# Kernel optimization log

Hardware: AMD Instinct MI355X
Metric: run time of the kernel (lower is better)

The kernel has to match this reference:

```python
import jax, jax.numpy as jnp
import numpy as np

N_NODES = 100000
N_EDGES = 1600000
BN_EPS = 1e-5

def gin_layer(h, src, dst, eps, w1, b1, w2, b2, gamma, beta, mean, var):
    # message passing: sum of source-node features at each target node
    agg = jax.ops.segment_sum(h[src], dst, num_segments=h.shape[0])  # [N, H]
    z = (1.0 + eps) * h + agg
    z = jax.nn.relu(z @ w1 + b1)
    z = jax.nn.relu(z @ w2 + b2)
    # BatchNorm1d in eval mode (running stats as params)
    return gamma * (z - mean) * jax.lax.rsqrt(var + BN_EPS) + beta

def setup_inputs() -> dict:
    key = jax.random.key(0)
    ks = jax.random.split(key, 12)
    H = 64
    s = lambda fan: 1.0 / np.sqrt(fan)
    inp = {
        "x": jax.random.normal(ks[0], (N_NODES, 128), jnp.float32),
        "edge_index": jax.random.randint(ks[1], (2, N_EDGES), 0, N_NODES, jnp.int64),
        "eps": jnp.zeros((3,), jnp.float32),
        "c1_w1": jax.random.normal(ks[2], (128, H), jnp.float32) * s(128),
        "c1_b1": jnp.zeros((H,), jnp.float32),
        "c1_w2": jax.random.normal(ks[3], (H, H), jnp.float32) * s(H),
        "c1_b2": jnp.zeros((H,), jnp.float32),
        "c1_gamma": jnp.ones((H,), jnp.float32),
        "c1_beta": jnp.zeros((H,), jnp.float32),
        "c1_mean": jnp.zeros((H,), jnp.float32),
        "c1_var": jnp.ones((H,), jnp.float32),
        "cw1": jax.random.normal(ks[4], (2, H, H), jnp.float32) * s(H),
        "cb1": jnp.zeros((2, H), jnp.float32),
        "cw2": jax.random.normal(ks[5], (2, H, H), jnp.float32) * s(H),
        "cb2": jnp.zeros((2, H), jnp.float32),
        "cgamma": jnp.ones((2, H), jnp.float32),
        "cbeta": jnp.zeros((2, H), jnp.float32),
        "cmean": jnp.zeros((2, H), jnp.float32),
        "cvar": jnp.ones((2, H), jnp.float32),
        "lin1_w": jax.random.normal(ks[6], (H, H), jnp.float32) * s(H),
        "lin1_b": jnp.zeros((H,), jnp.float32),
        "lin2_w": jax.random.normal(ks[7], (H, 40), jnp.float32) * s(H),
        "lin2_b": jnp.zeros((40,), jnp.float32),
    }
    return inp

def reference(x, edge_index, eps, c1_w1, c1_b1, c1_w2, c1_b2, c1_gamma, c1_beta,
              c1_mean, c1_var, cw1, cb1, cw2, cb2, cgamma, cbeta, cmean, cvar,
              lin1_w, lin1_b, lin2_w, lin2_b):
    src, dst = edge_index[0], edge_index[1]
    h = gin_layer(x, src, dst, eps[0], c1_w1, c1_b1, c1_w2, c1_b2,
                  c1_gamma, c1_beta, c1_mean, c1_var)
    for i in range(2):  # num_layers - 1 stacked GINConvs
        h = gin_layer(h, src, dst, eps[i + 1], cw1[i], cb1[i], cw2[i], cb2[i],
                      cgamma[i], cbeta[i], cmean[i], cvar[i])
    h = jax.nn.relu(h @ lin1_w + lin1_b)
    # dropout(p=0.5) is identity in eval mode
    return h @ lin2_w + lin2_b  # logits [N, num_classes]
```

## Files before the change

kernel.cpp:

```cpp
#include <hip/hip_runtime.h>

#define NN 100000
#define NE 1600000
#define BN_EPS 1e-5f
#define NCOARSE 98
#define SC_CH 2048

typedef unsigned int u32;
typedef unsigned short u16;

static constexpr size_t OFF_ROW  = 0;
static constexpr size_t OFF_CTRL = 512u * 1024;
static constexpr size_t OFF_CSR  = 1u << 20;
static constexpr size_t OFF_U    = 8u << 20;
static constexpr size_t OFF_P1   = OFF_U;
static constexpr size_t OFF_YB0  = OFF_U + (size_t)NN * 64 * 4;
static constexpr size_t OFF_YB1  = OFF_YB0 + (size_t)NN * 64 * 2;

__device__ __forceinline__ u16 f2bf(float f) {
  u32 u = __float_as_uint(f);
  return (u16)((u + 0x7fffu + ((u >> 16) & 1u)) >> 16);
}
__device__ __forceinline__ float bflo(u32 u) { return __uint_as_float(u << 16); }
__device__ __forceinline__ float bfhi(u32 u) { return __uint_as_float(u & 0xffff0000u); }
__device__ __forceinline__ u32 pkbf(float lo, float hi) {
  return (u32)f2bf(lo) | ((u32)f2bf(hi) << 16);
}

typedef __bf16 bf16x8 __attribute__((ext_vector_type(8)));
typedef float f32x4 __attribute__((ext_vector_type(4)));
union FragCvt { uint4 u; bf16x8 b; u16 s[8]; };
__device__ __forceinline__ bf16x8 frag_u16(const u16* p) {
  FragCvt c; c.u = *(const uint4*)p; return c.b;
}

__global__ void __launch_bounds__(256) k_hist_c(const int* __restrict__ dst,
                                                int* __restrict__ ch) {
  __shared__ int h[NCOARSE];
  if (threadIdx.x < NCOARSE) h[threadIdx.x] = 0;
  __syncthreads();
  int i = blockIdx.x * 256 + threadIdx.x, stride = gridDim.x * 256;
  for (; i < NE; i += stride) atomicAdd(&h[dst[i] >> 10], 1);
  __syncthreads();
  if (threadIdx.x < NCOARSE && h[threadIdx.x]) atomicAdd(&ch[threadIdx.x], h[threadIdx.x]);
}

__global__ void k_scan_c(const int* __restrict__ ch, int* __restrict__ coff,
                         int* __restrict__ ccur) {
  if (threadIdx.x == 0) {
    int acc = 0;
    for (int i = 0; i < NCOARSE; i++) { coff[i] = acc; ccur[i] = acc; acc += ch[i]; }
    coff[NCOARSE] = acc;
  }
}

__global__ void __launch_bounds__(256) k_scat1(const int* __restrict__ src,
                                               const int* __restrict__ dst,
                                               int* __restrict__ ccur,
                                               u32* __restrict__ pairs1) {
  __shared__ int h[NCOARSE], base[NCOARSE];
  int t = threadIdx.x;
  int e0 = blockIdx.x * SC_CH;
  if (t < NCOARSE) h[t] = 0;
  __syncthreads();
  int myc[8]; u32 mypk[8];
#pragma unroll
  for (int q = 0; q < 8; q++) {
    int e = e0 + q * 256 + t;
    if (e < NE) {
      int d = dst[e], s = src[e];
      myc[q] = d >> 10;
      mypk[q] = (u32)s | ((u32)(d & 1023) << 17);
      atomicAdd(&h[myc[q]], 1);
    } else myc[q] = -1;
  }
  __syncthreads();
  if (t < NCOARSE) {
    base[t] = (h[t] > 0) ? atomicAdd(&ccur[t], h[t]) : 0;
    h[t] = 0;
  }
  __syncthreads();
#pragma unroll
  for (int q = 0; q < 8; q++) {
    if (myc[q] >= 0) {
      int p = atomicAdd(&h[myc[q]], 1);
      pairs1[base[myc[q]] + p] = mypk[q];
    }
  }
}

__global__ void __launch_bounds__(256) k_fill3(const u32* __restrict__ pairs1,
                                               const int* __restrict__ coff,
                                               int* __restrict__ row,
                                               int* __restrict__ csr) {
  __shared__ int lcnt[1024];
  __shared__ int loff[1024];
  __shared__ int sd[256];
  __shared__ u32 stage[20480];
  int c = blockIdx.x, t = threadIdx.x;
  int es = coff[c], ee = coff[c + 1];
  int m = ee - es;
  int nbase = c << 10;
  int nodes_in = NN - nbase; if (nodes_in > 1024) nodes_in = 1024;
  for (int i = t; i < 1024; i += 256) lcnt[i] = 0;
  __syncthreads();
  for (int i = es + t; i < ee; i += 256)
    atomicAdd(&lcnt[(pairs1[i] >> 17) & 1023], 1);
  __syncthreads();
  int b4 = t * 4;
  int c0 = lcnt[b4], c1 = lcnt[b4 + 1], c2 = lcnt[b4 + 2], c3 = lcnt[b4 + 3];
  int s4 = c0 + c1 + c2 + c3;
  sd[t] = s4;
  __syncthreads();
  for (int o = 1; o < 256; o <<= 1) {
    int x = (t >= o) ? sd[t - o] : 0;
    __syncthreads();
    sd[t] += x;
    __syncthreads();
  }
  int run = sd[t] - s4;
  loff[b4] = run;     run += c0;
  loff[b4 + 1] = run; run += c1;
  loff[b4 + 2] = run; run += c2;
  loff[b4 + 3] = run;
  __syncthreads();
  for (int i = t; i < nodes_in; i += 256) row[nbase + i] = es + loff[i];
  if (c == NCOARSE - 1 && t == 0) row[NN] = NE;
  for (int i = t; i < 1024; i += 256) lcnt[i] = loff[i];
  __syncthreads();
  if (m <= 20480) {
    for (int i = es + t; i < ee; i += 256) {
      u32 pk = pairs1[i];
      int p = atomicAdd(&lcnt[(pk >> 17) & 1023], 1);
      stage[p] = pk & 0x1FFFFu;
    }
    __syncthreads();
    for (int i = t; i < m; i += 256) csr[es + i] = (int)stage[i];
  } else {
    for (int i = es + t; i < ee; i += 256) {
      u32 pk = pairs1[i];
      int p = atomicAdd(&lcnt[(pk >> 17) & 1023], 1);
      csr[es + p] = (int)(pk & 0x1FFFFu);
    }
  }
}

__global__ void __launch_bounds__(256) k_gemm_x_mfma(const float* __restrict__ x,
                                                     const float* __restrict__ w,
                                                     u16* __restrict__ yb) {
  __shared__ __align__(16) u16 wT[64][136];
  __shared__ __align__(16) u16 ht[4][32][72];
  int tid = threadIdx.x;
  for (int idx = tid; idx < 8192; idx += 256) {
    int k = idx >> 6, n = idx & 63;
    wT[n][k] = f2bf(w[idx]);
  }
  __syncthreads();
  int wid = tid >> 6, lane = tid & 63;
  int grp = blockIdx.x * 4 + wid;
  if (grp >= NN / 32) return;
  int g0 = grp * 32;
  int mrow = lane & 15;
  int kc8 = (lane >> 4) * 8;
  int q4 = (lane >> 4) * 4;
  bf16x8 a[2][4];
#pragma unroll
  for (int mt = 0; mt < 2; mt++) {
    const float* xr = x + (size_t)(g0 + mt * 16 + mrow) * 128;
#pragma unroll
    for (int kc = 0; kc < 4; kc++) {
      float4 v0 = *(const float4*)(xr + kc * 32 + kc8);
      float4 v1 = *(const float4*)(xr + kc * 32 + kc8 + 4);
      FragCvt fc;
      fc.s[0] = f2bf(v0.x); fc.s[1] = f2bf(v0.y); fc.s[2] = f2bf(v0.z); fc.s[3] = f2bf(v0.w);
      fc.s[4] = f2bf(v1.x); fc.s[5] = f2bf(v1.y); fc.s[6] = f2bf(v1.z); fc.s[7] = f2bf(v1.w);
      a[mt][kc] = fc.b;
    }
  }
  f32x4 zero = {0.f, 0.f, 0.f, 0.f};
  f32x4 acc[2][4];
#pragma unroll
  for (int nt = 0; nt < 4; nt++) {
    bf16x8 bf[4];
#pragma unroll
    for (int kc = 0; kc < 4; kc++)
      bf[kc] = frag_u16(&wT[nt * 16 + mrow][kc * 32 + kc8]);
#pragma unroll
    for (int mt = 0; mt < 2; mt++) {
      f32x4 c = __builtin_amdgcn_mfma_f32_16x16x32_bf16(a[mt][0], bf[0], zero, 0, 0, 0);
      c = __builtin_amdgcn_mfma_f32_16x16x32_bf16(a[mt][1], bf[1], c, 0, 0, 0);
      c = __builtin_amdgcn_mfma_f32_16x16x32_bf16(a[mt][2], bf[2], c, 0, 0, 0);
      c = __builtin_amdgcn_mfma_f32_16x16x32_bf16(a[mt][3], bf[3], c, 0, 0, 0);
      acc[mt][nt] = c;
    }
  }
#pragma unroll
  for (int mt = 0; mt < 2; mt++)
#pragma unroll
    for (int nt = 0; nt < 4; nt++)
#pragma unroll
      for (int r = 0; r < 4; r++)
        ht[wid][mt * 16 + q4 + r][nt * 16 + mrow] = f2bf(acc[mt][nt][r]);
  asm volatile("s_waitcnt lgkmcnt(0)" ::: "memory");
#pragma unroll
  for (int it = 0; it < 4; it++) {
    int idx = it * 64 + lane;
    int rw = idx >> 3, ch = idx & 7;
    uint4 v = *(const uint4*)&ht[wid][rw][ch * 8];
    *(uint4*)(yb + (size_t)(g0 + rw) * 64 + ch * 8) = v;
  }
}

__global__ void __launch_bounds__(256) k_agg(
    const u16* __restrict__ yb, const int* __restrict__ row, const int* __restrict__ csr,
    const float* __restrict__ epsv, int ei, const float* __restrict__ b1,
    u16* __restrict__ ub) {
  int t = blockIdx.x * 256 + threadIdx.x;
  int n = t >> 3, g = t & 7;
  if (n >= NN) return;
  const u16* bp = yb + g * 8;
  float a0 = 0, a1 = 0, a2 = 0, a3 = 0, a4 = 0, a5 = 0, a6 = 0, a7 = 0;
  int rs = row[n], re = row[n + 1];
  int i = rs;
  for (; i + 8 <= re; i += 8) {
    uint4 v[8];
#pragma unroll
    for (int q = 0; q < 8; q++) {
      int s = csr[i + q];
      v[q] = *(const uint4*)(bp + (size_t)s * 64);
    }
#pragma unroll
    for (int q = 0; q < 8; q++) {
      a0 += bflo(v[q].x); a1 += bfhi(v[q].x); a2 += bflo(v[q].y); a3 += bfhi(v[q].y);
      a4 += bflo(v[q].z); a5 += bfhi(v[q].z); a6 += bflo(v[q].w); a7 += bfhi(v[q].w);
    }
  }
  for (; i + 4 <= re; i += 4) {
    uint4 v[4];
#pragma unroll
    for (int q = 0; q < 4; q++) {
      int s = csr[i + q];
      v[q] = *(const uint4*)(bp + (size_t)s * 64);
    }
#pragma unroll
    for (int q = 0; q < 4; q++) {
      a0 += bflo(v[q].x); a1 += bfhi(v[q].x); a2 += bflo(v[q].y); a3 += bfhi(v[q].y);
      a4 += bflo(v[q].z); a5 += bfhi(v[q].z); a6 += bflo(v[q].w); a7 += bfhi(v[q].w);
    }
  }
  for (; i < re; ++i) {
    int s = csr[i];
    uint4 v0 = *(const uint4*)(bp + (size_t)s * 64);
    a0 += bflo(v0.x); a1 += bfhi(v0.x); a2 += bflo(v0.y); a3 += bfhi(v0.y);
    a4 += bflo(v0.z); a5 += bfhi(v0.z); a6 += bflo(v0.w); a7 += bfhi(v0.w);
  }
  uint4 sv = *(const uint4*)(bp + (size_t)n * 64);
  float e1 = 1.0f + epsv[ei];
  const float* bb = b1 + g * 8;
  float r0 = fmaxf(fmaf(e1, bflo(sv.x), a0 + bb[0]), 0.f);
  float r1 = fmaxf(fmaf(e1, bfhi(sv.x), a1 + bb[1]), 0.f);
  float r2 = fmaxf(fmaf(e1, bflo(sv.y), a2 + bb[2]), 0.f);
  float r3 = fmaxf(fmaf(e1, bfhi(sv.y), a3 + bb[3]), 0.f);
  float r4 = fmaxf(fmaf(e1, bflo(sv.z), a4 + bb[4]), 0.f);
  float r5 = fmaxf(fmaf(e1, bfhi(sv.z), a5 + bb[5]), 0.f);
  float r6 = fmaxf(fmaf(e1, bflo(sv.w), a6 + bb[6]), 0.f);
  float r7 = fmaxf(fmaf(e1, bfhi(sv.w), a7 + bb[7]), 0.f);
  uint4 pk;
  pk.x = pkbf(r0, r1); pk.y = pkbf(r2, r3);
  pk.z = pkbf(r4, r5); pk.w = pkbf(r6, r7);
  *(uint4*)(ub + (size_t)n * 64 + g * 8) = pk;
}

__global__ void __launch_bounds__(256) k_mlp_mfma(
    const u16* __restrict__ ub, const float* __restrict__ w2, const float* __restrict__ b2,
    const float* __restrict__ gamma, const float* __restrict__ beta,
    const float* __restrict__ mean, const float* __restrict__ var,
    const float* __restrict__ wn, u16* __restrict__ yout) {
  __shared__ __align__(16) u16 w2T[64][72];
  __shared__ __align__(16) u16 wnT[64][72];
  __shared__ __align__(16) u16 ht[4][32][72];
  int tid = threadIdx.x;
  for (int idx = tid; idx < 4096; idx += 256) {
    int k = idx >> 6, n = idx & 63;
    w2T[n][k] = f2bf(w2[idx]);
    wnT[n][k] = f2bf(wn[idx]);
  }
  __syncthreads();
  int wid = tid >> 6, lane = tid & 63;
  int grp = blockIdx.x * 4 + wid;
  if (grp >= NN / 32) return;
  int g0 = grp * 32;
  int mrow = lane & 15;
  int kc8 = (lane >> 4) * 8;
  int q4 = (lane >> 4) * 4;
  float bb[4], gl[4], be[4], mn[4], rv[4];
#pragma unroll
  for (int nt = 0; nt < 4; nt++) {
    int j = nt * 16 + mrow;
    bb[nt] = b2[j]; gl[nt] = gamma[j]; be[nt] = beta[j]; mn[nt] = mean[j];
    rv[nt] = rsqrtf(var[j] + BN_EPS);
  }
  bf16x8 a[2][2];
#pragma unroll
  for (int mt = 0; mt < 2; mt++)
#pragma unroll
    for (int kc = 0; kc < 2; kc++)
      a[mt][kc] = frag_u16(ub + (size_t)(g0 + mt * 16 + mrow) * 64 + kc * 32 + kc8);
  f32x4 zero = {0.f, 0.f, 0.f, 0.f};
  f32x4 acc[2][4];
#pragma unroll
  for (int nt = 0; nt < 4; nt++) {
    bf16x8 b0 = frag_u16(&w2T[nt * 16 + mrow][kc8]);
    bf16x8 b1f = frag_u16(&w2T[nt * 16 + mrow][32 + kc8]);
#pragma unroll
    for (int mt = 0; mt < 2; mt++) {
      acc[mt][nt] = __builtin_amdgcn_mfma_f32_16x16x32_bf16(a[mt][0], b0, zero, 0, 0, 0);
      acc[mt][nt] = __builtin_amdgcn_mfma_f32_16x16x32_bf16(a[mt][1], b1f, acc[mt][nt], 0, 0, 0);
    }
  }
#pragma unroll
  for (int mt = 0; mt < 2; mt++)
#pragma unroll
    for (int nt = 0; nt < 4; nt++)
#pragma unroll
      for (int r = 0; r < 4; r++) {
        float v = fmaxf(acc[mt][nt][r] + bb[nt], 0.f);
        float h = fmaf(gl[nt] * (v - mn[nt]), rv[nt], be[nt]);
        ht[wid][mt * 16 + q4 + r][nt * 16 + mrow] = f2bf(h);
      }
  asm volatile("s_waitcnt lgkmcnt(0)" ::: "memory");
  bf16x8 a2[2][2];
#pragma unroll
  for (int mt = 0; mt < 2; mt++)
#pragma unroll
    for (int kc = 0; kc < 2; kc++)
      a2[mt][kc] = frag_u16(&ht[wid][mt * 16 + mrow][kc * 32 + kc8]);
  f32x4 ac2[2][4];
#pragma unroll
  for (int nt = 0; nt < 4; nt++) {
    bf16x8 b0 = frag_u16(&wnT[nt * 16 + mrow][kc8]);
    bf16x8 b1f = frag_u16(&wnT[nt * 16 + mrow][32 + kc8]);
#pragma unroll
    for (int mt = 0; mt < 2; mt++) {
      ac2[mt][nt] = __builtin_amdgcn_mfma_f32_16x16x32_bf16(a2[mt][0], b0, zero, 0, 0, 0);
      ac2[mt][nt] = __builtin_amdgcn_mfma_f32_16x16x32_bf16(a2[mt][1], b1f, ac2[mt][nt], 0, 0, 0);
    }
  }
  asm volatile("s_waitcnt lgkmcnt(0)" ::: "memory");
#pragma unroll
  for (int mt = 0; mt < 2; mt++)
#pragma unroll
    for (int nt = 0; nt < 4; nt++)
#pragma unroll
      for (int r = 0; r < 4; r++)
        ht[wid][mt * 16 + q4 + r][nt * 16 + mrow] = f2bf(ac2[mt][nt][r]);
  asm volatile("s_waitcnt lgkmcnt(0)" ::: "memory");
#pragma unroll
  for (int it = 0; it < 4; it++) {
    int idx = it * 64 + lane;
    int rw = idx >> 3, ch = idx & 7;
    uint4 v = *(const uint4*)&ht[wid][rw][ch * 8];
    *(uint4*)(yout + (size_t)(g0 + rw) * 64 + ch * 8) = v;
  }
}

__global__ void __launch_bounds__(256) k_mlp_final_mfma(
    const u16* __restrict__ ub, const float* __restrict__ w2, const float* __restrict__ b2,
    const float* __restrict__ gamma, const float* __restrict__ beta,
    const float* __restrict__ mean, const float* __restrict__ var,
    const float* __restrict__ l1w, const float* __restrict__ l1b,
    const float* __restrict__ l2w, const float* __restrict__ l2b,
    float* __restrict__ out) {
  __shared__ __align__(16) u16 w2T[64][72];
  __shared__ __align__(16) u16 l1T[64][72];
  __shared__ __align__(16) u16 l2T[48][72];
  __shared__ __align__(16) u16 ht[4][32][72];
  int tid = threadIdx.x;
  for (int idx = tid; idx < 4096; idx += 256) {
    int k = idx >> 6, n = idx & 63;
    w2T[n][k] = f2bf(w2[idx]);
    l1T[n][k] = f2bf(l1w[idx]);
  }
  for (int idx = tid; idx < 3072; idx += 256) {
    int n = idx >> 6, k = idx & 63;
    l2T[n][k] = f2bf((n < 40) ? l2w[k * 40 + n] : 0.f);
  }
  __syncthreads();
  int wid = tid >> 6, lane = tid & 63;
  int grp = blockIdx.x * 4 + wid;
  if (grp >= NN / 32) return;
  int g0 = grp * 32;
  int mrow = lane & 15;
  int kc8 = (lane >> 4) * 8;
  int q4 = (lane >> 4) * 4;
  float bb[4], gl[4], be[4], mn[4], rv[4], l1bv[4];
#pragma unroll
  for (int nt = 0; nt < 4; nt++) {
    int j = nt * 16 + mrow;
    bb[nt] = b2[j]; gl[nt] = gamma[j]; be[nt] = beta[j]; mn[nt] = mean[j];
    rv[nt] = rsqrtf(var[j] + BN_EPS); l1bv[nt] = l1b[j];
  }
  float l2bv[3];
#pragma unroll
  for (int nt = 0; nt < 3; nt++) {
    int j = nt * 16 + mrow;
    l2bv[nt] = (j < 40) ? l2b[j] : 0.f;
  }
  bf16x8 a[2][2];
#pragma unroll
  for (int mt = 0; mt < 2; mt++)
#pragma unroll
    for (int kc = 0; kc < 2; kc++)
      a[mt][kc] = frag_u16(ub + (size_t)(g0 + mt * 16 + mrow) * 64 + kc * 32 + kc8);
  f32x4 zero = {0.f, 0.f, 0.f, 0.f};
  f32x4 acc[2][4];
#pragma unroll
  for (int nt = 0; nt < 4; nt++) {
    bf16x8 b0 = frag_u16(&w2T[nt * 16 + mrow][kc8]);
    bf16x8 b1f = frag_u16(&w2T[nt * 16 + mrow][32 + kc8]);
#pragma unroll
    for (int mt = 0; mt < 2; mt++) {
      acc[mt][nt] = __builtin_amdgcn_mfma_f32_16x16x32_bf16(a[mt][0], b0, zero, 0, 0, 0);
      acc[mt][nt] = __builtin_amdgcn_mfma_f32_16x16x32_bf16(a[mt][1], b1f, acc[mt][nt], 0, 0, 0);
    }
  }
#pragma unroll
  for (int mt = 0; mt < 2; mt++)
#pragma unroll
    for (int nt = 0; nt < 4; nt++)
#pragma unroll
      for (int r = 0; r < 4; r++) {
        float v = fmaxf(acc[mt][nt][r] + bb[nt], 0.f);
        float h = fmaf(gl[nt] * (v - mn[nt]), rv[nt], be[nt]);
        ht[wid][mt * 16 + q4 + r][nt * 16 + mrow] = f2bf(h);
      }
  asm volatile("s_waitcnt lgkmcnt(0)" ::: "memory");
  bf16x8 a2[2][2];
#pragma unroll
  for (int mt = 0; mt < 2; mt++)
#pragma unroll
    for (int kc = 0; kc < 2; kc++)
      a2[mt][kc] = frag_u16(&ht[wid][mt * 16 + mrow][kc * 32 + kc8]);
  f32x4 ac2[2][4];
#pragma unroll
  for (int nt = 0; nt < 4; nt++) {
    bf16x8 b0 = frag_u16(&l1T[nt * 16 + mrow][kc8]);
    bf16x8 b1f = frag_u16(&l1T[nt * 16 + mrow][32 + kc8]);
#pragma unroll
    for (int mt = 0; mt < 2; mt++) {
      ac2[mt][nt] = __builtin_amdgcn_mfma_f32_16x16x32_bf16(a2[mt][0], b0, zero, 0, 0, 0);
      ac2[mt][nt] = __builtin_amdgcn_mfma_f32_16x16x32_bf16(a2[mt][1], b1f, ac2[mt][nt], 0, 0, 0);
    }
  }
  asm volatile("s_waitcnt lgkmcnt(0)" ::: "memory");
#pragma unroll
  for (int mt = 0; mt < 2; mt++)
#pragma unroll
    for (int nt = 0; nt < 4; nt++)
#pragma unroll
      for (int r = 0; r < 4; r++) {
        float f = fmaxf(ac2[mt][nt][r] + l1bv[nt], 0.f);
        ht[wid][mt * 16 + q4 + r][nt * 16 + mrow] = f2bf(f);
      }
  asm volatile("s_waitcnt lgkmcnt(0)" ::: "memory");
  bf16x8 a3[2][2];
#pragma unroll
  for (int mt = 0; mt < 2; mt++)
#pragma unroll
    for (int kc = 0; kc < 2; kc++)
      a3[mt][kc] = frag_u16(&ht[wid][mt * 16 + mrow][kc * 32 + kc8]);
  f32x4 ac3[2][3];
#pragma unroll
  for (int nt = 0; nt < 3; nt++) {
    bf16x8 b0 = frag_u16(&l2T[nt * 16 + mrow][kc8]);
    bf16x8 b1f = frag_u16(&l2T[nt * 16 + mrow][32 + kc8]);
#pragma unroll
    for (int mt = 0; mt < 2; mt++) {
      ac3[mt][nt] = __builtin_amdgcn_mfma_f32_16x16x32_bf16(a3[mt][0], b0, zero, 0, 0, 0);
      ac3[mt][nt] = __builtin_amdgcn_mfma_f32_16x16x32_bf16(a3[mt][1], b1f, ac3[mt][nt], 0, 0, 0);
    }
  }
#pragma unroll
  for (int mt = 0; mt < 2; mt++)
#pragma unroll
    for (int nt = 0; nt < 3; nt++) {
      int j = nt * 16 + mrow;
      if (j < 40) {
#pragma unroll
        for (int r = 0; r < 4; r++)
          out[(size_t)(g0 + mt * 16 + q4 + r) * 40 + j] = ac3[mt][nt][r] + l2bv[nt];
      }
    }
}

extern "C" void kernel_launch(void* const* d_in, const int* in_sizes, int n_in,
                              void* d_out, int out_size, void* d_ws, size_t ws_size,
                              hipStream_t stream) {
  const float* x   = (const float*)d_in[0];
  const int*   ei  = (const int*)d_in[1];
  const int*   src = ei;
  const int*   dst = ei + NE;
  const float* eps = (const float*)d_in[2];
  const float* c1_w1 = (const float*)d_in[3];
  const float* c1_b1 = (const float*)d_in[4];
  const float* c1_w2 = (const float*)d_in[5];
  const float* c1_b2 = (const float*)d_in[6];
  const float* c1_gamma = (const float*)d_in[7];
  const float* c1_beta  = (const float*)d_in[8];
  const float* c1_mean  = (const float*)d_in[9];
  const float* c1_var   = (const float*)d_in[10];
  const float* cw1 = (const float*)d_in[11];
  const float* cb1 = (const float*)d_in[12];
  const float* cw2 = (const float*)d_in[13];
  const float* cb2 = (const float*)d_in[14];
  const float* cgamma = (const float*)d_in[15];
  const float* cbeta  = (const float*)d_in[16];
  const float* cmean  = (const float*)d_in[17];
  const float* cvar   = (const float*)d_in[18];
  const float* lin1_w = (const float*)d_in[19];
  const float* lin1_b = (const float*)d_in[20];
  const float* lin2_w = (const float*)d_in[21];
  const float* lin2_b = (const float*)d_in[22];
  float* out = (float*)d_out;

  char* ws = (char*)d_ws;
  int* row  = (int*)(ws + OFF_ROW);
  int* ctrl = (int*)(ws + OFF_CTRL);
  int* ch   = ctrl;
  int* coff = ctrl + 128;
  int* ccur = ctrl + 256;
  int* csr  = (int*)(ws + OFF_CSR);
  u32* pairs1 = (u32*)(ws + OFF_P1);
  u16* ubuf = (u16*)(ws + OFF_U);
  u16* yb0  = (u16*)(ws + OFF_YB0);
  u16* yb1  = (u16*)(ws + OFF_YB1);

  hipMemsetAsync(ch, 0, NCOARSE * 4, stream);

  k_hist_c<<<512, 256, 0, stream>>>(dst, ch);
  k_scan_c<<<1, 64, 0, stream>>>(ch, coff, ccur);
  k_scat1<<<(NE + SC_CH - 1) / SC_CH, 256, 0, stream>>>(src, dst, ccur, pairs1);
  k_fill3<<<NCOARSE, 256, 0, stream>>>(pairs1, coff, row, csr);

  const int AGG_GRID = (NN * 8) / 256;
  const int MLP_GRID = (NN / 32 + 3) / 4;

  k_gemm_x_mfma<<<MLP_GRID, 256, 0, stream>>>(x, c1_w1, yb0);

  k_agg<<<AGG_GRID, 256, 0, stream>>>(yb0, row, csr, eps, 0, c1_b1, ubuf);
  k_mlp_mfma<<<MLP_GRID, 256, 0, stream>>>(ubuf, c1_w2, c1_b2,
                                           c1_gamma, c1_beta, c1_mean, c1_var,
                                           cw1, yb1);
  k_agg<<<AGG_GRID, 256, 0, stream>>>(yb1, row, csr, eps, 1, cb1, ubuf);
  k_mlp_mfma<<<MLP_GRID, 256, 0, stream>>>(ubuf, cw2, cb2,
                                           cgamma, cbeta, cmean, cvar,
                                           cw1 + 64 * 64, yb0);
  k_agg<<<AGG_GRID, 256, 0, stream>>>(yb0, row, csr, eps, 2, cb1 + 64, ubuf);
  k_mlp_final_mfma<<<MLP_GRID, 256, 0, stream>>>(ubuf, cw2 + 64 * 64, cb2 + 64,
                                                 cgamma + 64, cbeta + 64, cmean + 64, cvar + 64,
                                                 lin1_w, lin1_b, lin2_w, lin2_b,
                                                 out);
}
```

Baseline: 233.5 us.

## Fuse neighbor aggregation with per-layer MLP into a single GIN kernel

Merges the separate aggregation and MLP kernels into one kernel per layer. Each block gathers neighbor sums for 64 nodes into shared memory, then runs the two MFMA GEMMs with bias, ReLU and batch-norm on that tile. This removes the intermediate bf16 buffer round-trip through global memory and three kernel launches. In exchange each thread now gathers 16 features instead of 8, which means fewer threads per node and more registers per thread, and every block repeats the weight transpose into shared memory.

```diff
diff --git a/kernel.cpp b/kernel.cpp
--- a/kernel.cpp
+++ b/kernel.cpp
@@ -12,9 +12,8 @@
 static constexpr size_t OFF_ROW  = 0;
 static constexpr size_t OFF_CTRL = 512u * 1024;
 static constexpr size_t OFF_CSR  = 1u << 20;
-static constexpr size_t OFF_U    = 8u << 20;
-static constexpr size_t OFF_P1   = OFF_U;
-static constexpr size_t OFF_YB0  = OFF_U + (size_t)NN * 64 * 4;
+static constexpr size_t OFF_P1   = 8u << 20;
+static constexpr size_t OFF_YB0  = OFF_P1 + (size_t)NN * 64 * 4;
 static constexpr size_t OFF_YB1  = OFF_YB0 + (size_t)NN * 64 * 2;
 
 __device__ __forceinline__ u16 f2bf(float f) {
@@ -211,193 +210,301 @@
   }
 }
 
-__global__ void __launch_bounds__(256) k_agg(
+__global__ void __launch_bounds__(256, 4) k_gin_layer(
     const u16* __restrict__ yb, const int* __restrict__ row, const int* __restrict__ csr,
     const float* __restrict__ epsv, int ei, const float* __restrict__ b1,
-    u16* __restrict__ ub) {
-  int t = blockIdx.x * 256 + threadIdx.x;
-  int n = t >> 3, g = t & 7;
-  if (n >= NN) return;
-  const u16* bp = yb + g * 8;
-  float a0 = 0, a1 = 0, a2 = 0, a3 = 0, a4 = 0, a5 = 0, a6 = 0, a7 = 0;
-  int rs = row[n], re = row[n + 1];
-  int i = rs;
-  for (; i + 8 <= re; i += 8) {
-    uint4 v[8];
-#pragma unroll
-    for (int q = 0; q < 8; q++) {
-      int s = csr[i + q];
-      v[q] = *(const uint4*)(bp + (size_t)s * 64);
-    }
-#pragma unroll
-    for (int q = 0; q < 8; q++) {
-      a0 += bflo(v[q].x); a1 += bfhi(v[q].x); a2 += bflo(v[q].y); a3 += bfhi(v[q].y);
-      a4 += bflo(v[q].z); a5 += bfhi(v[q].z); a6 += bflo(v[q].w); a7 += bfhi(v[q].w);
-    }
-  }
-  for (; i + 4 <= re; i += 4) {
-    uint4 v[4];
-#pragma unroll
-    for (int q = 0; q < 4; q++) {
-      int s = csr[i + q];
-      v[q] = *(const uint4*)(bp + (size_t)s * 64);
-    }
-#pragma unroll
-    for (int q = 0; q < 4; q++) {
-      a0 += bflo(v[q].x); a1 += bfhi(v[q].x); a2 += bflo(v[q].y); a3 += bfhi(v[q].y);
-      a4 += bflo(v[q].z); a5 += bfhi(v[q].z); a6 += bflo(v[q].w); a7 += bfhi(v[q].w);
-    }
-  }
-  for (; i < re; ++i) {
-    int s = csr[i];
-    uint4 v0 = *(const uint4*)(bp + (size_t)s * 64);
-    a0 += bflo(v0.x); a1 += bfhi(v0.x); a2 += bflo(v0.y); a3 += bfhi(v0.y);
-    a4 += bflo(v0.z); a5 += bfhi(v0.z); a6 += bflo(v0.w); a7 += bfhi(v0.w);
-  }
-  uint4 sv = *(const uint4*)(bp + (size_t)n * 64);
-  float e1 = 1.0f + epsv[ei];
-  const float* bb = b1 + g * 8;
-  float r0 = fmaxf(fmaf(e1, bflo(sv.x), a0 + bb[0]), 0.f);
-  float r1 = fmaxf(fmaf(e1, bfhi(sv.x), a1 + bb[1]), 0.f);
-  float r2 = fmaxf(fmaf(e1, bflo(sv.y), a2 + bb[2]), 0.f);
-  float r3 = fmaxf(fmaf(e1, bfhi(sv.y), a3 + bb[3]), 0.f);
-  float r4 = fmaxf(fmaf(e1, bflo(sv.z), a4 + bb[4]), 0.f);
-  float r5 = fmaxf(fmaf(e1, bfhi(sv.z), a5 + bb[5]), 0.f);
-  float r6 = fmaxf(fmaf(e1, bflo(sv.w), a6 + bb[6]), 0.f);
-  float r7 = fmaxf(fmaf(e1, bfhi(sv.w), a7 + bb[7]), 0.f);
-  uint4 pk;
-  pk.x = pkbf(r0, r1); pk.y = pkbf(r2, r3);
-  pk.z = pkbf(r4, r5); pk.w = pkbf(r6, r7);
-  *(uint4*)(ub + (size_t)n * 64 + g * 8) = pk;
-}
-
-__global__ void __launch_bounds__(256) k_mlp_mfma(
-    const u16* __restrict__ ub, const float* __restrict__ w2, const float* __restrict__ b2,
+    const float* __restrict__ w2, const float* __restrict__ b2,
     const float* __restrict__ gamma, const float* __restrict__ beta,
     const float* __restrict__ mean, const float* __restrict__ var,
     const float* __restrict__ wn, u16* __restrict__ yout) {
-  __shared__ __align__(16) u16 w2T[64][72];
-  __shared__ __align__(16) u16 wnT[64][72];
-  __shared__ __align__(16) u16 ht[4][32][72];
+  __shared__ __align__(16) u16 wA[64][72];
+  __shared__ __align__(16) u16 wB[64][72];
+  __shared__ __align__(16) u16 buf[64][72];
   int tid = threadIdx.x;
   for (int idx = tid; idx < 4096; idx += 256) {
     int k = idx >> 6, n = idx & 63;
-    w2T[n][k] = f2bf(w2[idx]);
-    wnT[n][k] = f2bf(wn[idx]);
-  }
-  __syncthreads();
-  int wid = tid >> 6, lane = tid & 63;
-  int grp = blockIdx.x * 4 + wid;
-  if (grp >= NN / 32) return;
-  int g0 = grp * 32;
-  int mrow = lane & 15;
-  int kc8 = (lane >> 4) * 8;
-  int q4 = (lane >> 4) * 4;
-  float bb[4], gl[4], be[4], mn[4], rv[4];
+    wA[n][k] = f2bf(w2[idx]);
+    wB[n][k] = f2bf(wn[idx]);
+  }
+  __syncthreads();
+
+  int ln = tid >> 2, q = tid & 3;
+  int n = blockIdx.x * 64 + ln;
+  int fb = q * 16;
+  float a[16];
+#pragma unroll
+  for (int j = 0; j < 16; j++) a[j] = 0.f;
+  if (n < NN) {
+    const u16* bp = yb + fb;
+    int rs = row[n], re = row[n + 1];
+    int i = rs;
+    for (; i + 8 <= re; i += 8) {
+      uint4 v[16];
+#pragma unroll
+      for (int p = 0; p < 8; p++) {
+        const u16* rp = bp + (size_t)csr[i + p] * 64;
+        v[2 * p]     = *(const uint4*)rp;
+        v[2 * p + 1] = *(const uint4*)(rp + 8);
+      }
+#pragma unroll
+      for (int p = 0; p < 8; p++) {
+        uint4 v0 = v[2 * p], v1 = v[2 * p + 1];
+        a[0] += bflo(v0.x); a[1] += bfhi(v0.x); a[2] += bflo(v0.y); a[3] += bfhi(v0.y);
+        a[4] += bflo(v0.z); a[5] += bfhi(v0.z); a[6] += bflo(v0.w); a[7] += bfhi(v0.w);
+        a[8] += bflo(v1.x); a[9] += bfhi(v1.x); a[10] += bflo(v1.y); a[11] += bfhi(v1.y);
+        a[12] += bflo(v1.z); a[13] += bfhi(v1.z); a[14] += bflo(v1.w); a[15] += bfhi(v1.w);
+      }
+    }
+    for (; i + 4 <= re; i += 4) {
+      uint4 v[8];
+#pragma unroll
+      for (int p = 0; p < 4; p++) {
+        const u16* rp = bp + (size_t)csr[i + p] * 64;
+        v[2 * p]     = *(const uint4*)rp;
+        v[2 * p + 1] = *(const uint4*)(rp + 8);
+      }
+#pragma unroll
+      for (int p = 0; p < 4; p++) {
+        uint4 v0 = v[2 * p], v1 = v[2 * p + 1];
+        a[0] += bflo(v0.x); a[1] += bfhi(v0.x); a[2] += bflo(v0.y); a[3] += bfhi(v0.y);
+        a[4] += bflo(v0.z); a[5] += bfhi(v0.z); a[6] += bflo(v0.w); a[7] += bfhi(v0.w);
+        a[8] += bflo(v1.x); a[9] += bfhi(v1.x); a[10] += bflo(v1.y); a[11] += bfhi(v1.y);
+        a[12] += bflo(v1.z); a[13] += bfhi(v1.z); a[14] += bflo(v1.w); a[15] += bfhi(v1.w);
+      }
+    }
+    for (; i < re; ++i) {
+      const u16* rp = bp + (size_t)csr[i] * 64;
+      uint4 v0 = *(const uint4*)rp;
+      uint4 v1 = *(const uint4*)(rp + 8);
+      a[0] += bflo(v0.x); a[1] += bfhi(v0.x); a[2] += bflo(v0.y); a[3] += bfhi(v0.y);
+      a[4] += bflo(v0.z); a[5] += bfhi(v0.z); a[6] += bflo(v0.w); a[7] += bfhi(v0.w);
+      a[8] += bflo(v1.x); a[9] += bfhi(v1.x); a[10] += bflo(v1.y); a[11] += bfhi(v1.y);
+      a[12] += bflo(v1.z); a[13] += bfhi(v1.z); a[14] += bflo(v1.w); a[15] += bfhi(v1.w);
+    }
+    const u16* sp = yb + (size_t)n * 64 + fb;
+    uint4 s0 = *(const uint4*)sp, s1 = *(const uint4*)(sp + 8);
+    float e1 = 1.0f + epsv[ei];
+    float4 bb0 = *(const float4*)(b1 + fb);
+    float4 bb1 = *(const float4*)(b1 + fb + 4);
+    float4 bb2 = *(const float4*)(b1 + fb + 8);
+    float4 bb3 = *(const float4*)(b1 + fb + 12);
+    float r[16];
+    r[0] = fmaxf(fmaf(e1, bflo(s0.x), a[0] + bb0.x), 0.f);
+    r[1] = fmaxf(fmaf(e1, bfhi(s0.x), a[1] + bb0.y), 0.f);
+    r[2] = fmaxf(fmaf(e1, bflo(s0.y), a[2] + bb0.z), 0.f);
+    r[3] = fmaxf(fmaf(e1, bfhi(s0.y), a[3] + bb0.w), 0.f);
+    r[4] = fmaxf(fmaf(e1, bflo(s0.z), a[4] + bb1.x), 0.f);
+    r[5] = fmaxf(fmaf(e1, bfhi(s0.z), a[5] + bb1.y), 0.f);
+    r[6] = fmaxf(fmaf(e1, bflo(s0.w), a[6] + bb1.z), 0.f);
+    r[7] = fmaxf(fmaf(e1, bfhi(s0.w), a[7] + bb1.w), 0.f);
+    r[8] = fmaxf(fmaf(e1, bflo(s1.x), a[8] + bb2.x), 0.f);
+    r[9] = fmaxf(fmaf(e1, bfhi(s1.x), a[9] + bb2.y), 0.f);
+    r[10] = fmaxf(fmaf(e1, bflo(s1.y), a[10] + bb2.z), 0.f);
+    r[11] = fmaxf(fmaf(e1, bfhi(s1.y), a[11] + bb2.w), 0.f);
+    r[12] = fmaxf(fmaf(e1, bflo(s1.z), a[12] + bb3.x), 0.f);
+    r[13] = fmaxf(fmaf(e1, bfhi(s1.z), a[13] + bb3.y), 0.f);
+    r[14] = fmaxf(fmaf(e1, bflo(s1.w), a[14] + bb3.z), 0.f);
+    r[15] = fmaxf(fmaf(e1, bfhi(s1.w), a[15] + bb3.w), 0.f);
+    uint4 p0, p1;
+    p0.x = pkbf(r[0], r[1]);  p0.y = pkbf(r[2], r[3]);
+    p0.z = pkbf(r[4], r[5]);  p0.w = pkbf(r[6], r[7]);
+    p1.x = pkbf(r[8], r[9]);  p1.y = pkbf(r[10], r[11]);
+    p1.z = pkbf(r[12], r[13]); p1.w = pkbf(r[14], r[15]);
+    *(uint4*)&buf[ln][fb] = p0;
+    *(uint4*)&buf[ln][fb + 8] = p1;
+  } else {
+    uint4 z = {0, 0, 0, 0};
+    *(uint4*)&buf[ln][fb] = z;
+    *(uint4*)&buf[ln][fb + 8] = z;
+  }
+
+  int wv = tid >> 6, lane = tid & 63;
+  int mrow = lane & 15, kc8 = (lane >> 4) * 8, q4 = (lane >> 4) * 4;
+  int r0 = wv * 16;
+  int gn0 = blockIdx.x * 64 + r0;
+  float bbv[4], gl[4], be[4], mn[4], rv[4];
 #pragma unroll
   for (int nt = 0; nt < 4; nt++) {
     int j = nt * 16 + mrow;
-    bb[nt] = b2[j]; gl[nt] = gamma[j]; be[nt] = beta[j]; mn[nt] = mean[j];
+    bbv[nt] = b2[j]; gl[nt] = gamma[j]; be[nt] = beta[j]; mn[nt] = mean[j];
     rv[nt] = rsqrtf(var[j] + BN_EPS);
   }
-  bf16x8 a[2][2];
-#pragma unroll
-  for (int mt = 0; mt < 2; mt++)
-#pragma unroll
-    for (int kc = 0; kc < 2; kc++)
-      a[mt][kc] = frag_u16(ub + (size_t)(g0 + mt * 16 + mrow) * 64 + kc * 32 + kc8);
+  asm volatile("s_waitcnt lgkmcnt(0)" ::: "memory");
+  bf16x8 af[2];
+  af[0] = frag_u16(&buf[r0 + mrow][kc8]);
+  af[1] = frag_u16(&buf[r0 + mrow][32 + kc8]);
   f32x4 zero = {0.f, 0.f, 0.f, 0.f};
-  f32x4 acc[2][4];
+  f32x4 acc[4];
 #pragma unroll
   for (int nt = 0; nt < 4; nt++) {
-    bf16x8 b0 = frag_u16(&w2T[nt * 16 + mrow][kc8]);
-    bf16x8 b1f = frag_u16(&w2T[nt * 16 + mrow][32 + kc8]);
-#pragma unroll
-    for (int mt = 0; mt < 2; mt++) {
-      acc[mt][nt] = __builtin_amdgcn_mfma_f32_16x16x32_bf16(a[mt][0], b0, zero, 0, 0, 0);
-      acc[mt][nt] = __builtin_amdgcn_mfma_f32_16x16x32_bf16(a[mt][1], b1f, acc[mt][nt], 0, 0, 0);
-    }
-  }
-#pragma unroll
-  for (int mt = 0; mt < 2; mt++)
-#pragma unroll
-    for (int nt = 0; nt < 4; nt++)
-#pragma unroll
-      for (int r = 0; r < 4; r++) {
-        float v = fmaxf(acc[mt][nt][r] + bb[nt], 0.f);
-        float h = fmaf(gl[nt] * (v - mn[nt]), rv[nt], be[nt]);
-        ht[wid][mt * 16 + q4 + r][nt * 16 + mrow] = f2bf(h);
-      }
-  asm volatile("s_waitcnt lgkmcnt(0)" ::: "memory");
-  bf16x8 a2[2][2];
-#pragma unroll
-  for (int mt = 0; mt < 2; mt++)
-#pragma unroll
-    for (int kc = 0; kc < 2; kc++)
-      a2[mt][kc] = frag_u16(&ht[wid][mt * 16 + mrow][kc * 32 + kc8]);
-  f32x4 ac2[2][4];
+    bf16x8 b0 = frag_u16(&wA[nt * 16 + mrow][kc8]);
+    bf16x8 b1f = frag_u16(&wA[nt * 16 + mrow][32 + kc8]);
+    acc[nt] = __builtin_amdgcn_mfma_f32_16x16x32_bf16(af[0], b0, zero, 0, 0, 0);
+    acc[nt] = __builtin_amdgcn_mfma_f32_16x16x32_bf16(af[1], b1f, acc[nt], 0, 0, 0);
+  }
+#pragma unroll
+  for (int nt = 0; nt < 4; nt++)
+#pragma unroll
+    for (int r = 0; r < 4; r++) {
+      float v = fmaxf(acc[nt][r] + bbv[nt], 0.f);
+      float h = fmaf(gl[nt] * (v - mn[nt]), rv[nt], be[nt]);
+      buf[r0 + q4 + r][nt * 16 + mrow] = f2bf(h);
+    }
+  asm volatile("s_waitcnt lgkmcnt(0)" ::: "memory");
+  bf16x8 a2[2];
+  a2[0] = frag_u16(&buf[r0 + mrow][kc8]);
+  a2[1] = frag_u16(&buf[r0 + mrow][32 + kc8]);
+  f32x4 ac2[4];
 #pragma unroll
   for (int nt = 0; nt < 4; nt++) {
-    bf16x8 b0 = frag_u16(&wnT[nt * 16 + mrow][kc8]);
-    bf16x8 b1f = frag_u16(&wnT[nt * 16 + mrow][32 + kc8]);
-#pragma unroll
-    for (int mt = 0; mt < 2; mt++) {
-      ac2[mt][nt] = __builtin_amdgcn_mfma_f32_16x16x32_bf16(a2[mt][0], b0, zero, 0, 0, 0);
-      ac2[mt][nt] = __builtin_amdgcn_mfma_f32_16x16x32_bf16(a2[mt][1], b1f, ac2[mt][nt], 0, 0, 0);
-    }
-  }
-  asm volatile("s_waitcnt lgkmcnt(0)" ::: "memory");
-#pragma unroll
-  for (int mt = 0; mt < 2; mt++)
-#pragma unroll
-    for (int nt = 0; nt < 4; nt++)
-#pragma unroll
-      for (int r = 0; r < 4; r++)
-        ht[wid][mt * 16 + q4 + r][nt * 16 + mrow] = f2bf(ac2[mt][nt][r]);
-  asm volatile("s_waitcnt lgkmcnt(0)" ::: "memory");
-#pragma unroll
-  for (int it = 0; it < 4; it++) {
+    bf16x8 b0 = frag_u16(&wB[nt * 16 + mrow][kc8]);
+    bf16x8 b1f = frag_u16(&wB[nt * 16 + mrow][32 + kc8]);
+    ac2[nt] = __builtin_amdgcn_mfma_f32_16x16x32_bf16(a2[0], b0, zero, 0, 0, 0);
+    ac2[nt] = __builtin_amdgcn_mfma_f32_16x16x32_bf16(a2[1], b1f, ac2[nt], 0, 0, 0);
+  }
+  asm volatile("s_waitcnt lgkmcnt(0)" ::: "memory");
+#pragma unroll
+  for (int nt = 0; nt < 4; nt++)
+#pragma unroll
+    for (int r = 0; r < 4; r++)
+      buf[r0 + q4 + r][nt * 16 + mrow] = f2bf(ac2[nt][r]);
+  asm volatile("s_waitcnt lgkmcnt(0)" ::: "memory");
+#pragma unroll
+  for (int it = 0; it < 2; it++) {
     int idx = it * 64 + lane;
     int rw = idx >> 3, ch = idx & 7;
-    uint4 v = *(const uint4*)&ht[wid][rw][ch * 8];
-    *(uint4*)(yout + (size_t)(g0 + rw) * 64 + ch * 8) = v;
-  }
-}
-
-__global__ void __launch_bounds__(256) k_mlp_final_mfma(
-    const u16* __restrict__ ub, const float* __restrict__ w2, const float* __restrict__ b2,
+    int gn = gn0 + rw;
+    if (gn < NN) {
+      uint4 v = *(const uint4*)&buf[r0 + rw][ch * 8];
+      *(uint4*)(yout + (size_t)gn * 64 + ch * 8) = v;
+    }
+  }
+}
+
+__global__ void __launch_bounds__(256, 4) k_gin_final(
+    const u16* __restrict__ yb, const int* __restrict__ row, const int* __restrict__ csr,
+    const float* __restrict__ epsv, int ei, const float* __restrict__ b1,
+    const float* __restrict__ w2, const float* __restrict__ b2,
     const float* __restrict__ gamma, const float* __restrict__ beta,
     const float* __restrict__ mean, const float* __restrict__ var,
     const float* __restrict__ l1w, const float* __restrict__ l1b,
     const float* __restrict__ l2w, const float* __restrict__ l2b,
     float* __restrict__ out) {
-  __shared__ __align__(16) u16 w2T[64][72];
-  __shared__ __align__(16) u16 l1T[64][72];
-  __shared__ __align__(16) u16 l2T[48][72];
-  __shared__ __align__(16) u16 ht[4][32][72];
+  __shared__ __align__(16) u16 wA[64][72];
+  __shared__ __align__(16) u16 wH[64][72];
+  __shared__ __align__(16) u16 wO[48][72];
+  __shared__ __align__(16) u16 buf[64][72];
   int tid = threadIdx.x;
   for (int idx = tid; idx < 4096; idx += 256) {
     int k = idx >> 6, n = idx & 63;
-    w2T[n][k] = f2bf(w2[idx]);
-    l1T[n][k] = f2bf(l1w[idx]);
+    wA[n][k] = f2bf(w2[idx]);
+    wH[n][k] = f2bf(l1w[idx]);
   }
   for (int idx = tid; idx < 3072; idx += 256) {
     int n = idx >> 6, k = idx & 63;
-    l2T[n][k] = f2bf((n < 40) ? l2w[k * 40 + n] : 0.f);
-  }
-  __syncthreads();
-  int wid = tid >> 6, lane = tid & 63;
-  int grp = blockIdx.x * 4 + wid;
-  if (grp >= NN / 32) return;
-  int g0 = grp * 32;
-  int mrow = lane & 15;
-  int kc8 = (lane >> 4) * 8;
-  int q4 = (lane >> 4) * 4;
-  float bb[4], gl[4], be[4], mn[4], rv[4], l1bv[4];
+    wO[n][k] = f2bf((n < 40) ? l2w[k * 40 + n] : 0.f);
+  }
+  __syncthreads();
+
+  int ln = tid >> 2, q = tid & 3;
+  int n = blockIdx.x * 64 + ln;
+  int fb = q * 16;
+  float a[16];
+#pragma unroll
+  for (int j = 0; j < 16; j++) a[j] = 0.f;
+  if (n < NN) {
+    const u16* bp = yb + fb;
+    int rs = row[n], re = row[n + 1];
+    int i = rs;
+    for (; i + 8 <= re; i += 8) {
+      uint4 v[16];
+#pragma unroll
+      for (int p = 0; p < 8; p++) {
+        const u16* rp = bp + (size_t)csr[i + p] * 64;
+        v[2 * p]     = *(const uint4*)rp;
+        v[2 * p + 1] = *(const uint4*)(rp + 8);
+      }
+#pragma unroll
+      for (int p = 0; p < 8; p++) {
+        uint4 v0 = v[2 * p], v1 = v[2 * p + 1];
+        a[0] += bflo(v0.x); a[1] += bfhi(v0.x); a[2] += bflo(v0.y); a[3] += bfhi(v0.y);
+        a[4] += bflo(v0.z); a[5] += bfhi(v0.z); a[6] += bflo(v0.w); a[7] += bfhi(v0.w);
+        a[8] += bflo(v1.x); a[9] += bfhi(v1.x); a[10] += bflo(v1.y); a[11] += bfhi(v1.y);
+        a[12] += bflo(v1.z); a[13] += bfhi(v1.z); a[14] += bflo(v1.w); a[15] += bfhi(v1.w);
+      }
+    }
+    for (; i + 4 <= re; i += 4) {
+      uint4 v[8];
+#pragma unroll
+      for (int p = 0; p < 4; p++) {
+        const u16* rp = bp + (size_t)csr[i + p] * 64;
+        v[2 * p]     = *(const uint4*)rp;
+        v[2 * p + 1] = *(const uint4*)(rp + 8);
+      }
+#pragma unroll
+      for (int p = 0; p < 4; p++) {
+        uint4 v0 = v[2 * p], v1 = v[2 * p + 1];
+        a[0] += bflo(v0.x); a[1] += bfhi(v0.x); a[2] += bflo(v0.y); a[3] += bfhi(v0.y);
+        a[4] += bflo(v0.z); a[5] += bfhi(v0.z); a[6] += bflo(v0.w); a[7] += bfhi(v0.w);
+        a[8] += bflo(v1.x); a[9] += bfhi(v1.x); a[10] += bflo(v1.y); a[11] += bfhi(v1.y);
+        a[12] += bflo(v1.z); a[13] += bfhi(v1.z); a[14] += bflo(v1.w); a[15] += bfhi(v1.w);
+      }
+    }
+    for (; i < re; ++i) {
+      const u16* rp = bp + (size_t)csr[i] * 64;
+      uint4 v0 = *(const uint4*)rp;
+      uint4 v1 = *(const uint4*)(rp + 8);
+      a[0] += bflo(v0.x); a[1] += bfhi(v0.x); a[2] += bflo(v0.y); a[3] += bfhi(v0.y);
+      a[4] += bflo(v0.z); a[5] += bfhi(v0.z); a[6] += bflo(v0.w); a[7] += bfhi(v0.w);
+      a[8] += bflo(v1.x); a[9] += bfhi(v1.x); a[10] += bflo(v1.y); a[11] += bfhi(v1.y);
+      a[12] += bflo(v1.z); a[13] += bfhi(v1.z); a[14] += bflo(v1.w); a[15] += bfhi(v1.w);
+    }
+    const u16* sp = yb + (size_t)n * 64 + fb;
+    uint4 s0 = *(const uint4*)sp, s1 = *(const uint4*)(sp + 8);
+    float e1 = 1.0f + epsv[ei];
+    float4 bb0 = *(const float4*)(b1 + fb);
+    float4 bb1 = *(const float4*)(b1 + fb + 4);
+    float4 bb2 = *(const float4*)(b1 + fb + 8);
+    float4 bb3 = *(const float4*)(b1 + fb + 12);
+    float r[16];
+    r[0] = fmaxf(fmaf(e1, bflo(s0.x), a[0] + bb0.x), 0.f);
+    r[1] = fmaxf(fmaf(e1, bfhi(s0.x), a[1] + bb0.y), 0.f);
+    r[2] = fmaxf(fmaf(e1, bflo(s0.y), a[2] + bb0.z), 0.f);
+    r[3] = fmaxf(fmaf(e1, bfhi(s0.y), a[3] + bb0.w), 0.f);
+    r[4] = fmaxf(fmaf(e1, bflo(s0.z), a[4] + bb1.x), 0.f);
+    r[5] = fmaxf(fmaf(e1, bfhi(s0.z), a[5] + bb1.y), 0.f);
+    r[6] = fmaxf(fmaf(e1, bflo(s0.w), a[6] + bb1.z), 0.f);
+    r[7] = fmaxf(fmaf(e1, bfhi(s0.w), a[7] + bb1.w), 0.f);
+    r[8] = fmaxf(fmaf(e1, bflo(s1.x), a[8] + bb2.x), 0.f);
+    r[9] = fmaxf(fmaf(e1, bfhi(s1.x), a[9] + bb2.y), 0.f);
+    r[10] = fmaxf(fmaf(e1, bflo(s1.y), a[10] + bb2.z), 0.f);
+    r[11] = fmaxf(fmaf(e1, bfhi(s1.y), a[11] + bb2.w), 0.f);
+    r[12] = fmaxf(fmaf(e1, bflo(s1.z), a[12] + bb3.x), 0.f);
+    r[13] = fmaxf(fmaf(e1, bfhi(s1.z), a[13] + bb3.y), 0.f);
+    r[14] = fmaxf(fmaf(e1, bflo(s1.w), a[14] + bb3.z), 0.f);
+    r[15] = fmaxf(fmaf(e1, bfhi(s1.w), a[15] + bb3.w), 0.f);
+    uint4 p0, p1;
+    p0.x = pkbf(r[0], r[1]);  p0.y = pkbf(r[2], r[3]);
+    p0.z = pkbf(r[4], r[5]);  p0.w = pkbf(r[6], r[7]);
+    p1.x = pkbf(r[8], r[9]);  p1.y = pkbf(r[10], r[11]);
+    p1.z = pkbf(r[12], r[13]); p1.w = pkbf(r[14], r[15]);
+    *(uint4*)&buf[ln][fb] = p0;
+    *(uint4*)&buf[ln][fb + 8] = p1;
+  } else {
+    uint4 z = {0, 0, 0, 0};
+    *(uint4*)&buf[ln][fb] = z;
+    *(uint4*)&buf[ln][fb + 8] = z;
+  }
+
+  int wv = tid >> 6, lane = tid & 63;
+  int mrow = lane & 15, kc8 = (lane >> 4) * 8, q4 = (lane >> 4) * 4;
+  int r0 = wv * 16;
+  int gn0 = blockIdx.x * 64 + r0;
+  float bbv[4], gl[4], be[4], mn[4], rv[4], l1bv[4];
 #pragma unroll
   for (int nt = 0; nt < 4; nt++) {
     int j = nt * 16 + mrow;
-    bb[nt] = b2[j]; gl[nt] = gamma[j]; be[nt] = beta[j]; mn[nt] = mean[j];
+    bbv[nt] = b2[j]; gl[nt] = gamma[j]; be[nt] = beta[j]; mn[nt] = mean[j];
     rv[nt] = rsqrtf(var[j] + BN_EPS); l1bv[nt] = l1b[j];
   }
   float l2bv[3];
@@ -406,91 +513,70 @@
     int j = nt * 16 + mrow;
     l2bv[nt] = (j < 40) ? l2b[j] : 0.f;
   }
-  bf16x8 a[2][2];
-#pragma unroll
-  for (int mt = 0; mt < 2; mt++)
-#pragma unroll
-    for (int kc = 0; kc < 2; kc++)
-      a[mt][kc] = frag_u16(ub + (size_t)(g0 + mt * 16 + mrow) * 64 + kc * 32 + kc8);
+  asm volatile("s_waitcnt lgkmcnt(0)" ::: "memory");
+  bf16x8 af[2];
+  af[0] = frag_u16(&buf[r0 + mrow][kc8]);
+  af[1] = frag_u16(&buf[r0 + mrow][32 + kc8]);
   f32x4 zero = {0.f, 0.f, 0.f, 0.f};
-  f32x4 acc[2][4];
+  f32x4 acc[4];
 #pragma unroll
   for (int nt = 0; nt < 4; nt++) {
-    bf16x8 b0 = frag_u16(&w2T[nt * 16 + mrow][kc8]);
-    bf16x8 b1f = frag_u16(&w2T[nt * 16 + mrow][32 + kc8]);
-#pragma unroll
-    for (int mt = 0; mt < 2; mt++) {
-      acc[mt][nt] = __builtin_amdgcn_mfma_f32_16x16x32_bf16(a[mt][0], b0, zero, 0, 0, 0);
-      acc[mt][nt] = __builtin_amdgcn_mfma_f32_16x16x32_bf16(a[mt][1], b1f, acc[mt][nt], 0, 0, 0);
-    }
-  }
-#pragma unroll
-  for (int mt = 0; mt < 2; mt++)
-#pragma unroll
-    for (int nt = 0; nt < 4; nt++)
+    bf16x8 b0 = frag_u16(&wA[nt * 16 + mrow][kc8]);
+    bf16x8 b1f = frag_u16(&wA[nt * 16 + mrow][32 + kc8]);
+    acc[nt] = __builtin_amdgcn_mfma_f32_16x16x32_bf16(af[0], b0, zero, 0, 0, 0);
+    acc[nt] = __builtin_amdgcn_mfma_f32_16x16x32_bf16(af[1], b1f, acc[nt], 0, 0, 0);
+  }
+#pragma unroll
+  for (int nt = 0; nt < 4; nt++)
+#pragma unroll
+    for (int r = 0; r < 4; r++) {
+      float v = fmaxf(acc[nt][r] + bbv[nt], 0.f);
+      float h = fmaf(gl[nt] * (v - mn[nt]), rv[nt], be[nt]);
+      buf[r0 + q4 + r][nt * 16 + mrow] = f2bf(h);
+    }
+  asm volatile("s_waitcnt lgkmcnt(0)" ::: "memory");
+  bf16x8 a2[2];
+  a2[0] = frag_u16(&buf[r0 + mrow][kc8]);
+  a2[1] = frag_u16(&buf[r0 + mrow][32 + kc8]);
+  f32x4 ac2[4];
+#pragma unroll
+  for (int nt = 0; nt < 4; nt++) {
+    bf16x8 b0 = frag_u16(&wH[nt * 16 + mrow][kc8]);
+    bf16x8 b1f = frag_u16(&wH[nt * 16 + mrow][32 + kc8]);
+    ac2[nt] = __builtin_amdgcn_mfma_f32_16x16x32_bf16(a2[0], b0, zero, 0, 0, 0);
+    ac2[nt] = __builtin_amdgcn_mfma_f32_16x16x32_bf16(a2[1], b1f, ac2[nt], 0, 0, 0);
+  }
+  asm volatile("s_waitcnt lgkmcnt(0)" ::: "memory");
+#pragma unroll
+  for (int nt = 0; nt < 4; nt++)
+#pragma unroll
+    for (int r = 0; r < 4; r++) {
+      float f = fmaxf(ac2[nt][r] + l1bv[nt], 0.f);
+      buf[r0 + q4 + r][nt * 16 + mrow] = f2bf(f);
+    }
+  asm volatile("s_waitcnt lgkmcnt(0)" ::: "memory");
+  bf16x8 a3[2];
+  a3[0] = frag_u16(&buf[r0 + mrow][kc8]);
+  a3[1] = frag_u16(&buf[r0 + mrow][32 + kc8]);
+  f32x4 ac3[3];
+#pragma unroll
+  for (int nt = 0; nt < 3; nt++) {
+    bf16x8 b0 = frag_u16(&wO[nt * 16 + mrow][kc8]);
+    bf16x8 b1f = frag_u16(&wO[nt * 16 + mrow][32 + kc8]);
+    ac3[nt] = __builtin_amdgcn_mfma_f32_16x16x32_bf16(a3[0], b0, zero, 0, 0, 0);
+    ac3[nt] = __builtin_amdgcn_mfma_f32_16x16x32_bf16(a3[1], b1f, ac3[nt], 0, 0, 0);
+  }
+#pragma unroll
+  for (int nt = 0; nt < 3; nt++) {
+    int j = nt * 16 + mrow;
+    if (j < 40) {
 #pragma unroll
       for (int r = 0; r < 4; r++) {
-        float v = fmaxf(acc[mt][nt][r] + bb[nt], 0.f);
-        float h = fmaf(gl[nt] * (v - mn[nt]), rv[nt], be[nt]);
-        ht[wid][mt * 16 + q4 + r][nt * 16 + mrow] = f2bf(h);
-      }
-  asm volatile("s_waitcnt lgkmcnt(0)" ::: "memory");
-  bf16x8 a2[2][2];
-#pragma unroll
-  for (int mt = 0; mt < 2; mt++)
-#pragma unroll
-    for (int kc = 0; kc < 2; kc++)
-      a2[mt][kc] = frag_u16(&ht[wid][mt * 16 + mrow][kc * 32 + kc8]);
-  f32x4 ac2[2][4];
-#pragma unroll
-  for (int nt = 0; nt < 4; nt++) {
-    bf16x8 b0 = frag_u16(&l1T[nt * 16 + mrow][kc8]);
-    bf16x8 b1f = frag_u16(&l1T[nt * 16 + mrow][32 + kc8]);
-#pragma unroll
-    for (int mt = 0; mt < 2; mt++) {
-      ac2[mt][nt] = __builtin_amdgcn_mfma_f32_16x16x32_bf16(a2[mt][0], b0, zero, 0, 0, 0);
-      ac2[mt][nt] = __builtin_amdgcn_mfma_f32_16x16x32_bf16(a2[mt][1], b1f, ac2[mt][nt], 0, 0, 0);
-    }
-  }
-  asm volatile("s_waitcnt lgkmcnt(0)" ::: "memory");
-#pragma unroll
-  for (int mt = 0; mt < 2; mt++)
-#pragma unroll
-    for (int nt = 0; nt < 4; nt++)
-#pragma unroll
-      for (int r = 0; r < 4; r++) {
-        float f = fmaxf(ac2[mt][nt][r] + l1bv[nt], 0.f);
-        ht[wid][mt * 16 + q4 + r][nt * 16 + mrow] = f2bf(f);
-      }
-  asm volatile("s_waitcnt lgkmcnt(0)" ::: "memory");
-  bf16x8 a3[2][2];
-#pragma unroll
-  for (int mt = 0; mt < 2; mt++)
-#pragma unroll
-    for (int kc = 0; kc < 2; kc++)
-      a3[mt][kc] = frag_u16(&ht[wid][mt * 16 + mrow][kc * 32 + kc8]);
-  f32x4 ac3[2][3];
-#pragma unroll
-  for (int nt = 0; nt < 3; nt++) {
-    bf16x8 b0 = frag_u16(&l2T[nt * 16 + mrow][kc8]);
-    bf16x8 b1f = frag_u16(&l2T[nt * 16 + mrow][32 + kc8]);
-#pragma unroll
-    for (int mt = 0; mt < 2; mt++) {
-      ac3[mt][nt] = __builtin_amdgcn_mfma_f32_16x16x32_bf16(a3[mt][0], b0, zero, 0, 0, 0);
-      ac3[mt][nt] = __builtin_amdgcn_mfma_f32_16x16x32_bf16(a3[mt][1], b1f, ac3[mt][nt], 0, 0, 0);
-    }
-  }
-#pragma unroll
-  for (int mt = 0; mt < 2; mt++)
-#pragma unroll
-    for (int nt = 0; nt < 3; nt++) {
-      int j = nt * 16 + mrow;
-      if (j < 40) {
-#pragma unroll
-        for (int r = 0; r < 4; r++)
-          out[(size_t)(g0 + mt * 16 + q4 + r) * 40 + j] = ac3[mt][nt][r] + l2bv[nt];
-      }
-    }
+        int gn = gn0 + q4 + r;
+        if (gn < NN) out[(size_t)gn * 40 + j] = ac3[nt][r] + l2bv[nt];
+      }
+    }
+  }
 }
 
 extern "C" void kernel_launch(void* const* d_in, const int* in_sizes, int n_in,
@@ -531,7 +617,6 @@
   int* ccur = ctrl + 256;
   int* csr  = (int*)(ws + OFF_CSR);
   u32* pairs1 = (u32*)(ws + OFF_P1);
-  u16* ubuf = (u16*)(ws + OFF_U);
   u16* yb0  = (u16*)(ws + OFF_YB0);
   u16* yb1  = (u16*)(ws + OFF_YB1);
 
@@ -542,22 +627,22 @@
   k_scat1<<<(NE + SC_CH - 1) / SC_CH, 256, 0, stream>>>(src, dst, ccur, pairs1);
   k_fill3<<<NCOARSE, 256, 0, stream>>>(pairs1, coff, row, csr);
 
-  const int AGG_GRID = (NN * 8) / 256;
   const int MLP_GRID = (NN / 32 + 3) / 4;
+  const int GIN_GRID = (NN + 63) / 64;
 
   k_gemm_x_mfma<<<MLP_GRID, 256, 0, stream>>>(x, c1_w1, yb0);
 
-  k_agg<<<AGG_GRID, 256, 0, stream>>>(yb0, row, csr, eps, 0, c1_b1, ubuf);
-  k_mlp_mfma<<<MLP_GRID, 256, 0, stream>>>(ubuf, c1_w2, c1_b2,
-                                           c1_gamma, c1_beta, c1_mean, c1_var,
-                                           cw1, yb1);
-  k_agg<<<AGG_GRID, 256, 0, stream>>>(yb1, row, csr, eps, 1, cb1, ubuf);
-  k_mlp_mfma<<<MLP_GRID, 256, 0, stream>>>(ubuf, cw2, cb2,
-                                           cgamma, cbeta, cmean, cvar,
-                                           cw1 + 64 * 64, yb0);
-  k_agg<<<AGG_GRID, 256, 0, stream>>>(yb0, row, csr, eps, 2, cb1 + 64, ubuf);
-  k_mlp_final_mfma<<<MLP_GRID, 256, 0, stream>>>(ubuf, cw2 + 64 * 64, cb2 + 64,
-                                                 cgamma + 64, cbeta + 64, cmean + 64, cvar + 64,
-                                                 lin1_w, lin1_b, lin2_w, lin2_b,
-                                                 out);
-}
+  k_gin_layer<<<GIN_GRID, 256, 0, stream>>>(yb0, row, csr, eps, 0, c1_b1,
+                                            c1_w2, c1_b2,
+                                            c1_gamma, c1_beta, c1_mean, c1_var,
+                                            cw1, yb1);
+  k_gin_layer<<<GIN_GRID, 256, 0, stream>>>(yb1, row, csr, eps, 1, cb1,
+                                            cw2, cb2,
+                                            cgamma, cbeta, cmean, cvar,
+                                            cw1 + 64 * 64, yb0);
+  k_gin_final<<<GIN_GRID, 256, 0, stream>>>(yb0, row, csr, eps, 2, cb1 + 64,
+                                            cw2 + 64 * 64, cb2 + 64,
+                                            cgamma + 64, cbeta + 64, cmean + 64, cvar + 64,
+                                            lin1_w, lin1_b, lin2_w, lin2_b,
+                                            out);
+}
```

Result: slower. 327.2 us (+40.1%).
